# Performance work log

Measured on AMD Instinct MI355X. Metric: run time of the kernel, lower is better.

## Reference

```python
import jax, jax.numpy as jnp
import numpy as np

B = 128          # batch
STATE = 128      # input_shape[0]
ACT = 32         # outputs_count
N = STATE + ACT  # graph nodes = inputs_count
E = 5120         # edges = N * avg_degree(32)
HID = 256        # hidden_count


def setup_inputs() -> dict:
    key = jax.random.key(0)
    ks = jax.random.split(key, 10)
    state = jax.random.normal(ks[0], (B, STATE), jnp.float32)
    action = jax.random.normal(ks[1], (B, ACT), jnp.float32)
    edge_index = jax.random.randint(ks[2], (2, E), 0, N, jnp.int64)
    # GConvSeq([N, HID, HID]) parameters (xavier-ish scale)
    W1 = jax.random.normal(ks[3], (N, HID), jnp.float32) / np.sqrt(N)
    b1 = jnp.zeros((HID,), jnp.float32)
    W2 = jax.random.normal(ks[4], (HID, HID), jnp.float32) / np.sqrt(HID)
    b2 = jnp.zeros((HID,), jnp.float32)
    # output Linear(hidden_count, input_shape[0])
    Wo = jax.random.normal(ks[5], (HID, STATE), jnp.float32) / np.sqrt(HID)
    bo = jnp.zeros((STATE,), jnp.float32)
    return {"state": state, "action": action, "edge_index": edge_index,
            "W1": W1, "b1": b1, "W2": W2, "b2": b2, "Wo": Wo, "bo": bo}


def reference(state, action, edge_index, W1, b1, W2, b2, Wo, bo):
    x = jnp.concatenate([state, action], axis=1)           # (B, N)
    src, dst = edge_index[0], edge_index[1]
    # dynamic graph mask: node i sees features of its in-neighbours (+ self)
    A = jnp.zeros((N, N), x.dtype).at[dst, src].set(1.0)
    A = A.at[jnp.arange(N), jnp.arange(N)].set(1.0)
    h = x[:, None, :] * A[None, :, :]                      # (B, N, N) masked node features
    deg = jnp.maximum(jnp.zeros((N,), x.dtype).at[dst].add(1.0), 1.0)

    def gconv(h, W, b):
        msgs = h[:, src, :]                                # (B, E, F) gather
        agg = jnp.zeros(h.shape, h.dtype).at[:, dst, :].add(msgs)  # scatter-add
        agg = agg / deg[None, :, None]                     # mean aggregation
        return jax.nn.relu(agg @ W + b)

    h = gconv(h, W1, b1)                                   # (B, N, HID)
    h = gconv(h, W2, b2)                                   # (B, N, HID)
    pooled = h.mean(axis=1)                                # (B, HID) readout
    y = pooled @ Wo + bo                                   # (B, STATE)
    return y + state
```

## Files before the change

kernel.cpp:

```cpp
#include <hip/hip_runtime.h>

#define NN 160
#define BB 128
#define HH 256
#define EE 5120
#define ST 128
#define AC 32
#define IH 80

typedef __attribute__((ext_vector_type(8))) short short8;
typedef __attribute__((ext_vector_type(4))) short bf16x4;
typedef unsigned short us;
typedef __attribute__((ext_vector_type(4))) float f32x4;

__device__ inline us f2b(float f) {
    unsigned u = __builtin_bit_cast(unsigned, f);
    unsigned r = (u + 0x7FFFu + ((u >> 16) & 1u)) >> 16;
    return (us)r;
}
__device__ inline float b2f(us h) {
    return __builtin_bit_cast(float, (unsigned)h << 16);
}

__global__ __launch_bounds__(256)
void k_pre(const int* __restrict__ ei, const float* __restrict__ W1,
           const float* __restrict__ W2, const float* __restrict__ state,
           const float* __restrict__ bo, us* __restrict__ Pb,
           us* __restrict__ Mb, us* __restrict__ W1t, us* __restrict__ W2t,
           float* __restrict__ out)
{
    const int bx = blockIdx.x, tid = threadIdx.x;
    if (bx < NN) {
        __shared__ int crow[NN];
        __shared__ unsigned abit[NN * NN / 32];
        __shared__ float invdeg;
        if (tid < NN) crow[tid] = 0;
        for (int i = tid; i < NN * NN / 32; i += 256) abit[i] = 0;
        __syncthreads();
        for (int e = tid; e < EE; e += 256) {
            int s = ei[e], d = ei[EE + e];
            int p = d * NN + s;
            atomicOr(&abit[p >> 5], 1u << (p & 31));
            if (d == bx) atomicAdd(&crow[s], 1);
        }
        if (tid < NN) {
            int p = tid * NN + tid;
            atomicOr(&abit[p >> 5], 1u << (p & 31));
        }
        __syncthreads();
        if (tid == 0) {
            int dg = 0;
            for (int j = 0; j < NN; j++) dg += crow[j];
            invdeg = 1.0f / (float)(dg < 1 ? 1 : dg);
        }
        __syncthreads();
        if (tid < NN) {
            int s = 0;
            for (int k = 0; k < NN; k++) {
                int p = k * NN + tid;
                if (abit[p >> 5] & (1u << (p & 31))) s += crow[k];
            }
            Pb[bx * NN + tid] = f2b((float)s * invdeg);
            Mb[bx * NN + tid] = f2b((float)crow[tid] * invdeg);
        }
    } else if (bx < NN + 160) {
        int idx = (bx - NN) * 256 + tid;
        int n = idx / NN, k = idx - n * NN;
        W1t[idx] = f2b(W1[k * HH + n]);
    } else if (bx < NN + 160 + 256) {
        int idx = (bx - NN - 160) * 256 + tid;
        int n = idx >> 8, k = idx & 255;
        W2t[idx] = f2b(W2[k * HH + n]);
    } else {
        int idx = (bx - NN - 160 - 256) * 256 + tid;
        out[idx] = state[idx] + bo[idx & 127];
    }
}

__global__ __launch_bounds__(1024, 4)
void k_mega(const us* __restrict__ Pb, const float* __restrict__ state,
            const float* __restrict__ action, const us* __restrict__ W1t,
            const float* __restrict__ b1, const us* __restrict__ Mb,
            const us* __restrict__ W2t, const float* __restrict__ b2,
            const float* __restrict__ Wo, float* __restrict__ out)
{
    __shared__ __align__(16) us SH[69888];
    __shared__ float xb[NN];
    us* Ys  = SH;
    us* ts  = SH;
    us* h1s = SH + 26880;
    float* pp  = (float*)&SH[21120];
    float* pts = (float*)&SH[23168];

    const int ihalf = blockIdx.x, b = blockIdx.y, i_base = ihalf * IH;
    const int tid = threadIdx.x, lane = tid & 63, w = tid >> 6;
    const int rl = lane & 15, kq = lane >> 4;
    const int wr = w >> 3, wc = w & 7;

    if (tid < NN) xb[tid] = (tid < ST) ? state[b * ST + tid]
                                       : action[b * AC + (tid - ST)];
    __syncthreads();

    for (int c = tid; c < 3200; c += 1024) {
        int r = c / 20, col = (c % 20) * 8;
        short8 p = *(const short8*)&Pb[r * NN + col];
        short8 y;
#pragma unroll
        for (int u = 0; u < 8; u++)
            y[u] = (short)f2b(b2f((us)p[u]) * xb[col + u]);
        *(short8*)&Ys[r * 168 + col] = y;
    }
    __syncthreads();

    for (int hh = 0; hh < 2; hh++) {
        f32x4 acc1[5];
#pragma unroll
        for (int f = 0; f < 5; f++) acc1[f] = f32x4{0.f, 0.f, 0.f, 0.f};

        const us* w1row = W1t + (size_t)(hh * 128 + wc * 16 + rl) * NN + kq * 8;
#pragma unroll
        for (int kk = 0; kk < 5; kk++) {
            short8 bv = *(const short8*)&w1row[kk * 32];
            short8 af[5];
#pragma unroll
            for (int f = 0; f < 5; f++)
                af[f] = *(const short8*)&Ys[(wr * 80 + f * 16 + rl) * 168 + kk * 32 + kq * 8];
#pragma unroll
            for (int f = 0; f < 5; f++)
                acc1[f] = __builtin_amdgcn_mfma_f32_16x16x32_bf16(
                    af[f], bv, acc1[f], 0, 0, 0);
        }
        {
            int h = hh * 128 + wc * 16 + rl;
            float bias = b1[h];
#pragma unroll
            for (int f = 0; f < 5; f++) {
                int i0 = wr * 80 + f * 16 + kq * 4;
                bf16x4 v;
#pragma unroll
                for (int r = 0; r < 4; r++) {
                    float t = acc1[f][r] + bias;
                    v[r] = (short)f2b(t > 0.f ? t : 0.f);
                }
                *(bf16x4*)&h1s[h * 168 + i0] = v;
            }
        }
    }
    __syncthreads();

    {
        f32x4 acc2[5];
#pragma unroll
        for (int j = 0; j < 5; j++) acc2[j] = f32x4{0.f, 0.f, 0.f, 0.f};

#pragma unroll
        for (int kk = 0; kk < 5; kk++) {
            short8 a = *(const short8*)&h1s[(w * 16 + rl) * 168 + kk * 32 + kq * 8];
            short8 bfv[5];
#pragma unroll
            for (int j = 0; j < 5; j++)
                bfv[j] = *(const short8*)&Mb[(size_t)(i_base + j * 16 + rl) * NN + kk * 32 + kq * 8];
#pragma unroll
            for (int j = 0; j < 5; j++)
                acc2[j] = __builtin_amdgcn_mfma_f32_16x16x32_bf16(
                    a, bfv[j], acc2[j], 0, 0, 0);
        }
        {
            int h0 = w * 16 + kq * 4;
#pragma unroll
            for (int j = 0; j < 5; j++) {
                int ip = j * 16 + rl;
                bf16x4 v;
#pragma unroll
                for (int r = 0; r < 4; r++)
                    v[r] = (short)f2b(acc2[j][r]);
                *(bf16x4*)&ts[ip * 264 + h0] = v;
            }
        }
    }
    __syncthreads();

    f32x4 acc3[5];
#pragma unroll
    for (int f = 0; f < 5; f++) acc3[f] = f32x4{0.f, 0.f, 0.f, 0.f};
    {
        const us* w2row = W2t + (size_t)(w * 16 + rl) * HH + kq * 8;
#pragma unroll
        for (int kk = 0; kk < 8; kk++) {
            short8 bv = *(const short8*)&w2row[kk * 32];
            short8 af[5];
#pragma unroll
            for (int f = 0; f < 5; f++)
                af[f] = *(const short8*)&ts[(f * 16 + rl) * 264 + kk * 32 + kq * 8];
#pragma unroll
            for (int f = 0; f < 5; f++)
                acc3[f] = __builtin_amdgcn_mfma_f32_16x16x32_bf16(
                    af[f], bv, acc3[f], 0, 0, 0);
        }
    }

    {
        int h = w * 16 + rl;
        float bias = b2[h];
        float s = 0.f;
#pragma unroll
        for (int f = 0; f < 5; f++)
#pragma unroll
            for (int r = 0; r < 4; r++) {
                float v = acc3[f][r] + bias;
                s += v > 0.f ? v : 0.f;
            }
        pp[kq * HH + h] = s;
    }
    __syncthreads();
    {
        const int q = tid >> 7, s2 = tid & 127;
        float part = 0.f;
        for (int hx = q * 32; hx < q * 32 + 32; hx++) {
            float ph = pp[0 * HH + hx] + pp[1 * HH + hx] +
                       pp[2 * HH + hx] + pp[3 * HH + hx];
            part += ph * Wo[hx * ST + s2];
        }
        pts[q * ST + s2] = part;
        __syncthreads();
        if (tid < ST) {
            float o = 0.f;
#pragma unroll
            for (int qq = 0; qq < 8; qq++) o += pts[qq * ST + tid];
            atomicAdd(&out[b * ST + tid], o * (1.0f / NN));
        }
    }
}

extern "C" void kernel_launch(void* const* d_in, const int* in_sizes, int n_in,
                              void* d_out, int out_size, void* d_ws, size_t ws_size,
                              hipStream_t stream) {
    const float* state  = (const float*)d_in[0];
    const float* action = (const float*)d_in[1];
    const int*   ei     = (const int*)d_in[2];
    const float* W1     = (const float*)d_in[3];
    const float* b1     = (const float*)d_in[4];
    const float* W2     = (const float*)d_in[5];
    const float* b2     = (const float*)d_in[6];
    const float* Wo     = (const float*)d_in[7];
    const float* bo     = (const float*)d_in[8];
    float* out = (float*)d_out;

    char* ws = (char*)d_ws;
    size_t off = 0;
    auto alloc = [&](size_t bytes) {
        void* p = ws + off;
        off += (bytes + 255) & ~(size_t)255;
        return p;
    };
    us* Pb  = (us*)alloc(NN * NN * 2);
    us* Mb  = (us*)alloc(NN * NN * 2);
    us* W1t = (us*)alloc((size_t)HH * NN * 2);
    us* W2t = (us*)alloc((size_t)HH * HH * 2);

    k_pre<<<NN + 160 + 256 + 64, 256, 0, stream>>>(ei, W1, W2, state, bo,
                                                   Pb, Mb, W1t, W2t, out);
    {
        dim3 g(2, BB);
        k_mega<<<g, 1024, 0, stream>>>(Pb, state, action, W1t, b1, Mb, W2t, b2,
                                       Wo, out);
    }
}
```

Before: 33.13 us.

## Restructure GEMM1 per-wave tiling and stage Mb rows into shared memory

GEMM1 now gives each wave one 16-column slice of W1 across all 160 rows (10 MFMA accumulators) instead of looping twice over half-row tiles, so each W1 fragment is loaded once per wave. The Mb rows for GEMM2 are first copied into LDS with a cooperative load rather than being read directly from global inside the MFMA loop. The shared-memory regions are remapped to fit this, and the final readout reduction merges partials with LDS atomics. The trade-off is higher register pressure from 10 accumulators and an extra barrier plus copy step.

```diff
diff --git a/kernel.cpp b/kernel.cpp
--- a/kernel.cpp
+++ b/kernel.cpp
@@ -87,15 +87,15 @@
     __shared__ __align__(16) us SH[69888];
     __shared__ float xb[NN];
     us* Ys  = SH;
-    us* ts  = SH;
     us* h1s = SH + 26880;
-    float* pp  = (float*)&SH[21120];
-    float* pts = (float*)&SH[23168];
+    us* Mbs = SH;
+    us* ts  = SH + 26880;
+    float* pp  = (float*)&SH[13440];
+    float* pts = (float*)&SH[15488];
 
     const int ihalf = blockIdx.x, b = blockIdx.y, i_base = ihalf * IH;
     const int tid = threadIdx.x, lane = tid & 63, w = tid >> 6;
     const int rl = lane & 15, kq = lane >> 4;
-    const int wr = w >> 3, wc = w & 7;
 
     if (tid < NN) xb[tid] = (tid < ST) ? state[b * ST + tid]
                                        : action[b * AC + (tid - ST)];
@@ -112,70 +112,74 @@
     }
     __syncthreads();
 
-    for (int hh = 0; hh < 2; hh++) {
-        f32x4 acc1[5];
-#pragma unroll
-        for (int f = 0; f < 5; f++) acc1[f] = f32x4{0.f, 0.f, 0.f, 0.f};
-
-        const us* w1row = W1t + (size_t)(hh * 128 + wc * 16 + rl) * NN + kq * 8;
+    {
+        f32x4 acc1[10];
+#pragma unroll
+        for (int f = 0; f < 10; f++) acc1[f] = f32x4{0.f, 0.f, 0.f, 0.f};
+
+        const us* w1row = W1t + (size_t)(w * 16 + rl) * NN + kq * 8;
 #pragma unroll
         for (int kk = 0; kk < 5; kk++) {
             short8 bv = *(const short8*)&w1row[kk * 32];
-            short8 af[5];
-#pragma unroll
-            for (int f = 0; f < 5; f++)
-                af[f] = *(const short8*)&Ys[(wr * 80 + f * 16 + rl) * 168 + kk * 32 + kq * 8];
-#pragma unroll
-            for (int f = 0; f < 5; f++)
+            short8 af[10];
+#pragma unroll
+            for (int f = 0; f < 10; f++)
+                af[f] = *(const short8*)&Ys[(f * 16 + rl) * 168 + kk * 32 + kq * 8];
+#pragma unroll
+            for (int f = 0; f < 10; f++)
                 acc1[f] = __builtin_amdgcn_mfma_f32_16x16x32_bf16(
                     af[f], bv, acc1[f], 0, 0, 0);
         }
-        {
-            int h = hh * 128 + wc * 16 + rl;
-            float bias = b1[h];
-#pragma unroll
-            for (int f = 0; f < 5; f++) {
-                int i0 = wr * 80 + f * 16 + kq * 4;
-                bf16x4 v;
-#pragma unroll
-                for (int r = 0; r < 4; r++) {
-                    float t = acc1[f][r] + bias;
-                    v[r] = (short)f2b(t > 0.f ? t : 0.f);
-                }
-                *(bf16x4*)&h1s[h * 168 + i0] = v;
+        int h = w * 16 + rl;
+        float bias = b1[h];
+#pragma unroll
+        for (int f = 0; f < 10; f++) {
+            int i0 = f * 16 + kq * 4;
+            bf16x4 v;
+#pragma unroll
+            for (int r = 0; r < 4; r++) {
+                float t = acc1[f][r] + bias;
+                v[r] = (short)f2b(t > 0.f ? t : 0.f);
             }
-        }
-    }
-    __syncthreads();
-
-    {
-        f32x4 acc2[5];
-#pragma unroll
-        for (int j = 0; j < 5; j++) acc2[j] = f32x4{0.f, 0.f, 0.f, 0.f};
-
-#pragma unroll
-        for (int kk = 0; kk < 5; kk++) {
-            short8 a = *(const short8*)&h1s[(w * 16 + rl) * 168 + kk * 32 + kq * 8];
-            short8 bfv[5];
-#pragma unroll
-            for (int j = 0; j < 5; j++)
-                bfv[j] = *(const short8*)&Mb[(size_t)(i_base + j * 16 + rl) * NN + kk * 32 + kq * 8];
-#pragma unroll
-            for (int j = 0; j < 5; j++)
-                acc2[j] = __builtin_amdgcn_mfma_f32_16x16x32_bf16(
-                    a, bfv[j], acc2[j], 0, 0, 0);
-        }
-        {
-            int h0 = w * 16 + kq * 4;
-#pragma unroll
-            for (int j = 0; j < 5; j++) {
-                int ip = j * 16 + rl;
-                bf16x4 v;
-#pragma unroll
-                for (int r = 0; r < 4; r++)
-                    v[r] = (short)f2b(acc2[j][r]);
-                *(bf16x4*)&ts[ip * 264 + h0] = v;
-            }
+            *(bf16x4*)&h1s[h * 168 + i0] = v;
+        }
+    }
+    __syncthreads();
+
+    for (int c = tid; c < 1600; c += 1024) {
+        int r = c / 20, col = (c % 20) * 8;
+        *(short8*)&Mbs[r * 168 + col] =
+            *(const short8*)&Mb[(size_t)(i_base + r) * NN + col];
+    }
+    __syncthreads();
+
+    f32x4 acc2[5];
+#pragma unroll
+    for (int j = 0; j < 5; j++) acc2[j] = f32x4{0.f, 0.f, 0.f, 0.f};
+#pragma unroll
+    for (int kk = 0; kk < 5; kk++) {
+        short8 a = *(const short8*)&h1s[(w * 16 + rl) * 168 + kk * 32 + kq * 8];
+        short8 bfv[5];
+#pragma unroll
+        for (int j = 0; j < 5; j++)
+            bfv[j] = *(const short8*)&Mbs[(j * 16 + rl) * 168 + kk * 32 + kq * 8];
+#pragma unroll
+        for (int j = 0; j < 5; j++)
+            acc2[j] = __builtin_amdgcn_mfma_f32_16x16x32_bf16(
+                a, bfv[j], acc2[j], 0, 0, 0);
+    }
+    __syncthreads();
+
+    {
+        int h0 = w * 16 + kq * 4;
+#pragma unroll
+        for (int j = 0; j < 5; j++) {
+            int ip = j * 16 + rl;
+            bf16x4 v;
+#pragma unroll
+            for (int r = 0; r < 4; r++)
+                v[r] = (short)f2b(acc2[j][r]);
+            *(bf16x4*)&ts[ip * 264 + h0] = v;
         }
     }
     __syncthreads();
@@ -214,19 +218,20 @@
     }
     __syncthreads();
     {
-        const int q = tid >> 7, s2 = tid & 127;
+        const int q8 = tid >> 7, s128 = tid & 127;
         float part = 0.f;
-        for (int hx = q * 32; hx < q * 32 + 32; hx++) {
+        for (int hx = q8 * 32; hx < q8 * 32 + 32; hx++) {
             float ph = pp[0 * HH + hx] + pp[1 * HH + hx] +
                        pp[2 * HH + hx] + pp[3 * HH + hx];
-            part += ph * Wo[hx * ST + s2];
-        }
-        pts[q * ST + s2] = part;
+            part += ph * Wo[hx * ST + s128];
+        }
+        if (q8 < 4) pts[q8 * ST + s128] = part;
+        __syncthreads();
+        if (q8 >= 4) atomicAdd(&pts[(q8 - 4) * ST + s128], part);
         __syncthreads();
         if (tid < ST) {
-            float o = 0.f;
-#pragma unroll
-            for (int qq = 0; qq < 8; qq++) o += pts[qq * ST + tid];
+            float o = pts[0 * ST + tid] + pts[1 * ST + tid] +
+                      pts[2 * ST + tid] + pts[3 * ST + tid];
             atomicAdd(&out[b * ST + tid], o * (1.0f / NN));
         }
     }
```

Result: faster. 31.05 us (-6.3%).
